# Performance work log

Measured on AMD Instinct MI355X. Metric: run time of the kernel, lower is better.

The kernel has to match this reference:

```python
import jax, jax.numpy as jnp
import numpy as np

N = 50000   # nodes
E = 640000  # edges
IN, H, OUT = 128, 128, 64
BN_EPS = 1e-5


def setup_inputs() -> dict:
    key = jax.random.key(0)
    ks = jax.random.split(key, 16)
    inp = {}
    inp["x"] = jax.random.normal(ks[0], (N, IN), jnp.float32)
    inp["edge_index"] = jax.random.randint(ks[1], (2, E), 0, N, dtype=jnp.int32)
    # BatchNorm affine params (nontrivial so grads are informative)
    inp["bn_in_gamma"] = 1.0 + 0.1 * jax.random.normal(ks[2], (IN,), jnp.float32)
    inp["bn_in_beta"] = 0.1 * jax.random.normal(ks[3], (IN,), jnp.float32)
    inp["bn1_gamma"] = 1.0 + 0.1 * jax.random.normal(ks[4], (H,), jnp.float32)
    inp["bn1_beta"] = 0.1 * jax.random.normal(ks[5], (H,), jnp.float32)
    inp["bn2_gamma"] = 1.0 + 0.1 * jax.random.normal(ks[6], (OUT,), jnp.float32)
    inp["bn2_beta"] = 0.1 * jax.random.normal(ks[7], (OUT,), jnp.float32)
    # Linear / GCNConv weights (fan-in scaled)
    inp["proj_W"] = jax.random.normal(ks[8], (IN, H), jnp.float32) / np.sqrt(IN)
    inp["proj_b"] = jnp.zeros((H,), jnp.float32)
    inp["conv1_W"] = jax.random.normal(ks[9], (H, H), jnp.float32) / np.sqrt(H)
    inp["conv1_b"] = jnp.zeros((H,), jnp.float32)
    inp["conv2_W"] = jax.random.normal(ks[10], (H, OUT), jnp.float32) / np.sqrt(H)
    inp["conv2_b"] = jnp.zeros((OUT,), jnp.float32)
    return inp


def batchnorm(x, gamma, beta):
    # training-mode BN: batch statistics (biased variance), per-feature affine
    m = jnp.mean(x, axis=0)
    v = jnp.mean(jnp.square(x - m), axis=0)
    return (x - m) * jax.lax.rsqrt(v + BN_EPS) * gamma + beta


def gcn_conv(x, src, dst, W, b):
    # PyG GCNConv: y = D^{-1/2} (A + I) D^{-1/2} (x W) + b
    xw = x @ W                                    # [N, F_out]
    loops = jnp.arange(N, dtype=src.dtype)
    s = jnp.concatenate([src, loops])             # [E + N]
    d = jnp.concatenate([dst, loops])
    deg = jax.ops.segment_sum(jnp.ones_like(d, jnp.float32), d, num_segments=N)
    dinv = jnp.where(deg > 0, jax.lax.rsqrt(deg), 0.0)
    norm = dinv[s] * dinv[d]                      # [E + N]
    msgs = xw[s] * norm[:, None]                  # gather + per-edge scale
    out = jax.ops.segment_sum(msgs, d, num_segments=N)  # scatter-add
    return out + b


def reference(x, edge_index, bn_in_gamma, bn_in_beta, bn1_gamma, bn1_beta,
              bn2_gamma, bn2_beta, proj_W, proj_b, conv1_W, conv1_b,
              conv2_W, conv2_b):
    src, dst = edge_index[0], edge_index[1]
    h = batchnorm(x, bn_in_gamma, bn_in_beta)
    h = jax.nn.relu(h @ proj_W + proj_b)
    h = jax.nn.relu(batchnorm(gcn_conv(h, src, dst, conv1_W, conv1_b),
                              bn1_gamma, bn1_beta))
    # dropout: identity in eval mode
    out = batchnorm(gcn_conv(h, src, dst, conv2_W, conv2_b),
                    bn2_gamma, bn2_beta)
    return out
```

## Files before the change

### kernel.cpp

```cpp
#include <hip/hip_runtime.h>

#define NN 50000
#define NE 640000
#define BNEPS 1e-5f
#define NBANK 16
#define CAP 64

#define OFF_DINV 0
#define OFF_CURSOR 51200
#define OFF_ESRC 102400
#define OFF_WT0 1702400
#define OFF_WT1 1710592
#define OFF_WT2 1718784
#define OFF_STATS 1726976
#define OFF_B0 1737216
#define OFF_B1 8137216

typedef __attribute__((ext_vector_type(8))) __bf16 bf16x8;
typedef __attribute__((ext_vector_type(4))) float f32x4;

__device__ __forceinline__ float uplo(unsigned int u) {
  unsigned int v = u << 16;
  return __builtin_bit_cast(float, v);
}
__device__ __forceinline__ float uphi(unsigned int u) {
  unsigned int v = u & 0xffff0000u;
  return __builtin_bit_cast(float, v);
}
__device__ __forceinline__ unsigned int f2bf(float f) {
  unsigned int u = __builtin_bit_cast(unsigned int, f);
  return (u + 0x7fffu + ((u >> 16) & 1u)) >> 16;
}

__global__ __launch_bounds__(256) void prep_k(
    const float* __restrict__ W0, const float* __restrict__ W1,
    const float* __restrict__ W2, unsigned short* __restrict__ T0,
    unsigned short* __restrict__ T1, unsigned short* __restrict__ T2,
    int* __restrict__ cursor, float* __restrict__ stats) {
  const int bid = blockIdx.x;
  const int tid = threadIdx.x;
  if (bid < 160) {
    int f = bid * 256 + tid;
    if (f < 16384) {
      int k = f >> 7, n = f & 127;
      T0[n * 128 + k] = (unsigned short)f2bf(W0[f]);
    } else if (f < 32768) {
      int g = f - 16384;
      int k = g >> 7, n = g & 127;
      T1[n * 128 + k] = (unsigned short)f2bf(W1[g]);
    } else if (f < 40960) {
      int g = f - 32768;
      int k = g >> 6, n = g & 63;
      T2[n * 128 + k] = (unsigned short)f2bf(W2[g]);
    }
  } else if (bid < 356) {
    int i = (bid - 160) * 256 + tid;
    if (i < NN) cursor[i] = i * CAP;
  } else {
    int j = (bid - 356) * 256 + tid;
    stats[j] = 0.0f;
  }
}

template <int NC>
__device__ __forceinline__ void bn_stats_body(
    int sbid, int nsb, int tid, const float* __restrict__ A,
    float* __restrict__ sums, float* __restrict__ sqs, float (*rs)[NC],
    float (*rq)[NC]) {
  constexpr int CG = NC / 4;
  constexpr int RG = 256 / CG;
  const int tc = tid % CG;
  const int tr = tid / CG;
  float s0 = 0, s1 = 0, s2 = 0, s3 = 0, q0 = 0, q1 = 0, q2 = 0, q3 = 0;
  const int stride = nsb * RG;
  for (int r = sbid * RG + tr; r < NN; r += stride) {
    float4 v = *(const float4*)&A[(size_t)r * NC + tc * 4];
    s0 += v.x; s1 += v.y; s2 += v.z; s3 += v.w;
    q0 += v.x * v.x; q1 += v.y * v.y; q2 += v.z * v.z; q3 += v.w * v.w;
  }
  rs[tr][tc * 4] = s0; rs[tr][tc * 4 + 1] = s1;
  rs[tr][tc * 4 + 2] = s2; rs[tr][tc * 4 + 3] = s3;
  rq[tr][tc * 4] = q0; rq[tr][tc * 4 + 1] = q1;
  rq[tr][tc * 4 + 2] = q2; rq[tr][tc * 4 + 3] = q3;
  __syncthreads();
  if (tr == 0) {
    const int bank = (sbid & (NBANK - 1)) * NC;
    for (int j = 0; j < 4; ++j) {
      int c = tc * 4 + j;
      float ts = 0, tq = 0;
      for (int g = 0; g < RG; ++g) { ts += rs[g][c]; tq += rq[g][c]; }
      atomicAdd(&sums[bank + c], ts);
      atomicAdd(&sqs[bank + c], tq);
    }
  }
}

template <int NC>
__global__ __launch_bounds__(256) void bn_stats_k(const float* __restrict__ A,
                                                  float* __restrict__ sums,
                                                  float* __restrict__ sqs) {
  __shared__ float rs[256 / (NC / 4)][NC];
  __shared__ float rq[256 / (NC / 4)][NC];
  bn_stats_body<NC>(blockIdx.x, gridDim.x, threadIdx.x, A, sums, sqs, rs, rq);
}

__global__ __launch_bounds__(256) void bn_stats_bf_k(
    const unsigned short* __restrict__ Z, float* __restrict__ sums,
    float* __restrict__ sqs) {
  const int tc = threadIdx.x % 16;
  const int tr = threadIdx.x / 16;
  const int c = tc * 8;
  float s[8], q[8];
#pragma unroll
  for (int j = 0; j < 8; ++j) { s[j] = 0.f; q[j] = 0.f; }
  const int stride = gridDim.x * 16;
  for (int r = blockIdx.x * 16 + tr; r < NN; r += stride) {
    const uint4 p = *(const uint4*)&Z[(size_t)r * 128 + c];
    float e[8] = {uplo(p.x), uphi(p.x), uplo(p.y), uphi(p.y),
                  uplo(p.z), uphi(p.z), uplo(p.w), uphi(p.w)};
#pragma unroll
    for (int j = 0; j < 8; ++j) { s[j] += e[j]; q[j] += e[j] * e[j]; }
  }
  __shared__ float rs[16][128];
  __shared__ float rq[16][128];
#pragma unroll
  for (int j = 0; j < 8; ++j) { rs[tr][c + j] = s[j]; rq[tr][c + j] = q[j]; }
  __syncthreads();
  if (tr == 0) {
    const int bank = (blockIdx.x & (NBANK - 1)) * 128;
#pragma unroll
    for (int j = 0; j < 8; ++j) {
      float ts = 0.f, tq = 0.f;
      for (int g = 0; g < 16; ++g) { ts += rs[g][c + j]; tq += rq[g][c + j]; }
      atomicAdd(&sums[bank + c + j], ts);
      atomicAdd(&sqs[bank + c + j], tq);
    }
  }
}

template <int NC, int PRE, int EPI>
__device__ __forceinline__ void gemm_body(
    int bid, int tid, char* __restrict__ smem, float* __restrict__ af_s,
    float* __restrict__ bf_s, const void* __restrict__ Ain,
    const unsigned short* __restrict__ Wt, const float* __restrict__ bias,
    const float* __restrict__ sums, const float* __restrict__ sqs,
    const float* __restrict__ gamma, const float* __restrict__ beta,
    unsigned short* __restrict__ O1) {
  constexpr int TM = 64;
  constexpr int NTILES = NC / 16;
  constexpr int CSTR = NC + 4;
  const int row0 = bid * TM;

  if constexpr (PRE != 1) {
    if (tid < 128) {
      float s = 0.f, q = 0.f;
#pragma unroll
      for (int b = 0; b < NBANK; ++b) {
        s += sums[b * 128 + tid];
        q += sqs[b * 128 + tid];
      }
      float m = s * (1.0f / NN);
      float v = q * (1.0f / NN) - m * m;
      float a = gamma[tid] * rsqrtf(v + BNEPS);
      af_s[tid] = a;
      bf_s[tid] = beta[tid] - m * a;
    }
    __syncthreads();
    if constexpr (PRE == 0) {
      const float* A = (const float*)Ain;
      for (int f = tid; f < TM * 32; f += 256) {
        const int r = f >> 5;
        const int c4 = f & 31;
        const int rg = row0 + r;
        float4 v = make_float4(0.f, 0.f, 0.f, 0.f);
        if (rg < NN) {
          v = *(const float4*)&A[(size_t)rg * 128 + c4 * 4];
          const float4 a4 = *(const float4*)&af_s[c4 * 4];
          const float4 b4 = *(const float4*)&bf_s[c4 * 4];
          v.x = fmaf(a4.x, v.x, b4.x);
          v.y = fmaf(a4.y, v.y, b4.y);
          v.z = fmaf(a4.z, v.z, b4.z);
          v.w = fmaf(a4.w, v.w, b4.w);
        }
        uint2 wv;
        wv.x = f2bf(v.x) | (f2bf(v.y) << 16);
        wv.y = f2bf(v.z) | (f2bf(v.w) << 16);
        const int ba = (r * 256 + c4 * 8) ^ ((r & 7) << 4);
        *(uint2*)(smem + ba) = wv;
      }
    } else {
      const unsigned short* Ab = (const unsigned short*)Ain;
      for (int f = tid; f < TM * 16; f += 256) {
        const int r = f >> 4;
        const int c8 = f & 15;
        const int rg = row0 + r;
        uint4 w4 = make_uint4(0u, 0u, 0u, 0u);
        if (rg < NN) {
          const uint4 raw = *(const uint4*)&Ab[(size_t)rg * 128 + c8 * 8];
          const int cc = c8 * 8;
          float e[8] = {uplo(raw.x), uphi(raw.x), uplo(raw.y), uphi(raw.y),
                        uplo(raw.z), uphi(raw.z), uplo(raw.w), uphi(raw.w)};
          unsigned int p[4];
#pragma unroll
          for (int j = 0; j < 4; ++j) {
            float lo =
                fmaxf(fmaf(af_s[cc + 2 * j], e[2 * j], bf_s[cc + 2 * j]), 0.f);
            float hi = fmaxf(
                fmaf(af_s[cc + 2 * j + 1], e[2 * j + 1], bf_s[cc + 2 * j + 1]),
                0.f);
            p[j] = f2bf(lo) | (f2bf(hi) << 16);
          }
          w4 = make_uint4(p[0], p[1], p[2], p[3]);
        }
        const int ba = (r * 256 + c8 * 16) ^ ((r & 7) << 4);
        *(uint4*)(smem + ba) = w4;
      }
    }
    __syncthreads();
  }

  const int w = tid >> 6;
  const int l = tid & 63;
  const int lr = l & 15;
  const int lg = l >> 4;
  f32x4 acc[NTILES];
#pragma unroll
  for (int i = 0; i < NTILES; ++i) acc[i] = (f32x4){0.f, 0.f, 0.f, 0.f};
  const int arow = w * 16 + lr;
#pragma unroll
  for (int kt = 0; kt < 4; ++kt) {
    bf16x8 a;
    if constexpr (PRE == 1) {
      const unsigned short* Ab = (const unsigned short*)Ain;
      a = __builtin_bit_cast(
          bf16x8,
          *(const uint4*)&Ab[(size_t)(row0 + arow) * 128 + kt * 32 + lg * 8]);
    } else {
      const int ba = (arow * 256 + kt * 64 + lg * 16) ^ ((arow & 7) << 4);
      a = __builtin_bit_cast(bf16x8, *(const uint4*)(smem + ba));
    }
#pragma unroll
    for (int nt = 0; nt < NTILES; ++nt) {
      bf16x8 b = __builtin_bit_cast(
          bf16x8,
          *(const uint4*)&Wt[(size_t)(nt * 16 + lr) * 128 + kt * 32 + lg * 8]);
      acc[nt] = __builtin_amdgcn_mfma_f32_16x16x32_bf16(a, b, acc[nt], 0, 0, 0);
    }
  }

  float* Cl = (float*)smem;
  constexpr int CG = NC / 4;
  constexpr int RPH = CG / 8;
  const int tcx = tid % CG;
  const int trx = tid / CG;
  float4 b4 = make_float4(0.f, 0.f, 0.f, 0.f);
  if constexpr (EPI == 0) b4 = *(const float4*)&bias[tcx * 4];
#pragma unroll
  for (int half = 0; half < 2; ++half) {
    __syncthreads();
    if ((w >> 1) == half) {
#pragma unroll
      for (int nt = 0; nt < NTILES; ++nt)
#pragma unroll
        for (int r = 0; r < 4; ++r)
          Cl[((w & 1) * 16 + lg * 4 + r) * CSTR + nt * 16 + lr] = acc[nt][r];
    }
    __syncthreads();
#pragma unroll
    for (int i = 0; i < RPH; ++i) {
      const int rl = trx * RPH + i;
      const int rg = row0 + half * 32 + rl;
      if (rg < NN) {
        float4 v = *(const float4*)&Cl[rl * CSTR + tcx * 4];
        if (EPI == 0) {
          v.x = fmaxf(v.x + b4.x, 0.f);
          v.y = fmaxf(v.y + b4.y, 0.f);
          v.z = fmaxf(v.z + b4.z, 0.f);
          v.w = fmaxf(v.w + b4.w, 0.f);
        }
        uint2 o;
        o.x = f2bf(v.x) | (f2bf(v.y) << 16);
        o.y = f2bf(v.z) | (f2bf(v.w) << 16);
        *(uint2*)&O1[(size_t)rg * NC + tcx * 4] = o;
      }
    }
  }
}

__global__ __launch_bounds__(256) void stats_fill_k(
    const float* __restrict__ x, float* __restrict__ s0,
    float* __restrict__ q0, const int* __restrict__ src,
    const int* __restrict__ dst, int* __restrict__ cursor,
    unsigned short* __restrict__ esrc) {
  __shared__ float rs[8][128];
  __shared__ float rq[8][128];
  const int bid = blockIdx.x;
  if (bid < 1024) {
    bn_stats_body<128>(bid, 1024, threadIdx.x, x, s0, q0, rs, rq);
  } else {
    int e = (bid - 1024) * 256 + threadIdx.x;
    if (e < NE / 2) {
      int p = atomicAdd(&cursor[dst[e]], 1);
      esrc[p] = (unsigned short)src[e];
    }
  }
}

__global__ __launch_bounds__(256) void gemm1_fill_k(
    const float* __restrict__ x, const unsigned short* __restrict__ Wt0,
    const float* __restrict__ proj_b, const float* __restrict__ s0,
    const float* __restrict__ q0, const float* __restrict__ g0,
    const float* __restrict__ b0, unsigned short* __restrict__ H1bf,
    const int* __restrict__ src, const int* __restrict__ dst,
    int* __restrict__ cursor, unsigned short* __restrict__ esrc) {
  __shared__ __align__(16) char smem[17408];
  __shared__ float af_s[128];
  __shared__ float bf_s[128];
  const int bid = blockIdx.x;
  const int tid = threadIdx.x;
  if (bid < 782) {
    gemm_body<128, 0, 0>(bid, tid, smem, af_s, bf_s, x, Wt0, proj_b, s0, q0,
                         g0, b0, H1bf);
  } else {
    int e = NE / 2 + (bid - 782) * 256 + tid;
    if (e < NE) {
      int p = atomicAdd(&cursor[dst[e]], 1);
      esrc[p] = (unsigned short)src[e];
    }
  }
}

__global__ __launch_bounds__(256) void conv1_dinv_k(
    const unsigned short* __restrict__ H1bf,
    const unsigned short* __restrict__ Wt1, unsigned short* __restrict__ Ybf,
    const int* __restrict__ cursor, float* __restrict__ dinv) {
  __shared__ __align__(16) char smem[17408];
  __shared__ float af_s[128];
  __shared__ float bf_s[128];
  const int bid = blockIdx.x;
  const int tid = threadIdx.x;
  if (bid < 782) {
    gemm_body<128, 1, 2>(bid, tid, smem, af_s, bf_s, H1bf, Wt1, nullptr,
                         nullptr, nullptr, nullptr, nullptr, Ybf);
  } else {
    int i = (bid - 782) * 256 + tid;
    if (i < NN) {
      int d = cursor[i] - i * CAP;
      dinv[i] = rsqrtf((float)d + 1.0f);
    }
  }
}

template <int NC, int OUTBF>
__global__ __launch_bounds__(256) void gather_bf_k(
    const int* __restrict__ cursor, const unsigned short* __restrict__ esrc,
    const unsigned short* __restrict__ Y, const float* __restrict__ dinv,
    void* __restrict__ outp, const float* __restrict__ cb) {
  constexpr int CG = NC / 8;
  constexpr int RG = 256 / CG;
  const int tc = threadIdx.x % CG;
  const int tr = threadIdx.x / CG;
  const int n = blockIdx.x * RG + tr;
  if (n >= NN) return;
  const int c = tc * 8;
  const float dn = dinv[n];
  float a[8];
  {
    const uint4 p = *(const uint4*)&Y[(size_t)n * NC + c];
    a[0] = dn * uplo(p.x); a[1] = dn * uphi(p.x);
    a[2] = dn * uplo(p.y); a[3] = dn * uphi(p.y);
    a[4] = dn * uplo(p.z); a[5] = dn * uphi(p.z);
    a[6] = dn * uplo(p.w); a[7] = dn * uphi(p.w);
  }
  const int beg = n * CAP;
  const int end = cursor[n];
  int e = beg;
  for (; e + 2 <= end; e += 2) {
    const int s0 = esrc[e];
    const int s1 = esrc[e + 1];
    const float d0 = dinv[s0];
    const float d1 = dinv[s1];
    const uint4 q0 = *(const uint4*)&Y[(size_t)s0 * NC + c];
    const uint4 q1 = *(const uint4*)&Y[(size_t)s1 * NC + c];
    a[0] = fmaf(d0, uplo(q0.x), a[0]); a[1] = fmaf(d0, uphi(q0.x), a[1]);
    a[2] = fmaf(d0, uplo(q0.y), a[2]); a[3] = fmaf(d0, uphi(q0.y), a[3]);
    a[4] = fmaf(d0, uplo(q0.z), a[4]); a[5] = fmaf(d0, uphi(q0.z), a[5]);
    a[6] = fmaf(d0, uplo(q0.w), a[6]); a[7] = fmaf(d0, uphi(q0.w), a[7]);
    a[0] = fmaf(d1, uplo(q1.x), a[0]); a[1] = fmaf(d1, uphi(q1.x), a[1]);
    a[2] = fmaf(d1, uplo(q1.y), a[2]); a[3] = fmaf(d1, uphi(q1.y), a[3]);
    a[4] = fmaf(d1, uplo(q1.z), a[4]); a[5] = fmaf(d1, uphi(q1.z), a[5]);
    a[6] = fmaf(d1, uplo(q1.w), a[6]); a[7] = fmaf(d1, uphi(q1.w), a[7]);
  }
  if (e < end) {
    const int s0 = esrc[e];
    const float d0 = dinv[s0];
    const uint4 q0 = *(const uint4*)&Y[(size_t)s0 * NC + c];
    a[0] = fmaf(d0, uplo(q0.x), a[0]); a[1] = fmaf(d0, uphi(q0.x), a[1]);
    a[2] = fmaf(d0, uplo(q0.y), a[2]); a[3] = fmaf(d0, uphi(q0.y), a[3]);
    a[4] = fmaf(d0, uplo(q0.z), a[4]); a[5] = fmaf(d0, uphi(q0.z), a[5]);
    a[6] = fmaf(d0, uplo(q0.w), a[6]); a[7] = fmaf(d0, uphi(q0.w), a[7]);
  }
  float z[8];
#pragma unroll
  for (int j = 0; j < 8; ++j) z[j] = fmaf(dn, a[j], cb[c + j]);
  if constexpr (OUTBF == 1) {
    unsigned int p[4];
#pragma unroll
    for (int j = 0; j < 4; ++j)
      p[j] = f2bf(z[2 * j]) | (f2bf(z[2 * j + 1]) << 16);
    *(uint4*)&((unsigned short*)outp)[(size_t)n * NC + c] =
        make_uint4(p[0], p[1], p[2], p[3]);
  } else {
    float* Z = (float*)outp;
    *(float4*)&Z[(size_t)n * NC + c] = make_float4(z[0], z[1], z[2], z[3]);
    *(float4*)&Z[(size_t)n * NC + c + 4] = make_float4(z[4], z[5], z[6], z[7]);
  }
}

template <int NC, int PRE, int EPI>
__global__ __launch_bounds__(256) void mfma_gemm_k(
    const void* __restrict__ Ain, const unsigned short* __restrict__ Wt,
    const float* __restrict__ bias, const float* __restrict__ sums,
    const float* __restrict__ sqs, const float* __restrict__ gamma,
    const float* __restrict__ beta, unsigned short* __restrict__ O1) {
  constexpr int CBYTES = 32 * (NC + 4) * 4;
  constexpr int SMEM = (CBYTES > 16384) ? CBYTES : 16384;
  __shared__ __align__(16) char smem[SMEM];
  __shared__ float af_s[128];
  __shared__ float bf_s[128];
  gemm_body<NC, PRE, EPI>(blockIdx.x, threadIdx.x, smem, af_s, bf_s, Ain, Wt,
                          bias, sums, sqs, gamma, beta, O1);
}

__global__ __launch_bounds__(256) void final_k(
    const float* __restrict__ Z2, const float* __restrict__ s2,
    const float* __restrict__ q2, const float* __restrict__ gamma,
    const float* __restrict__ beta, float* __restrict__ out) {
  __shared__ float af_s[64];
  __shared__ float bf_s[64];
  if (threadIdx.x < 64) {
    float s = 0.f, q = 0.f;
#pragma unroll
    for (int b = 0; b < NBANK; ++b) {
      s += s2[b * 64 + threadIdx.x];
      q += q2[b * 64 + threadIdx.x];
    }
    float m = s * (1.0f / NN);
    float v = q * (1.0f / NN) - m * m;
    float a = gamma[threadIdx.x] * rsqrtf(v + BNEPS);
    af_s[threadIdx.x] = a;
    bf_s[threadIdx.x] = beta[threadIdx.x] - m * a;
  }
  __syncthreads();
  const int u = blockIdx.x * 256 + threadIdx.x;
  if (u >= NN * 16) return;
  const int r = u >> 4;
  const int c = (u & 15) * 4;
  float4 v = *(const float4*)&Z2[(size_t)r * 64 + c];
  const float4 a4 = *(const float4*)&af_s[c];
  const float4 b4 = *(const float4*)&bf_s[c];
  float4 o;
  o.x = fmaf(a4.x, v.x, b4.x);
  o.y = fmaf(a4.y, v.y, b4.y);
  o.z = fmaf(a4.z, v.z, b4.z);
  o.w = fmaf(a4.w, v.w, b4.w);
  *(float4*)&out[(size_t)r * 64 + c] = o;
}

extern "C" void kernel_launch(void* const* d_in, const int* in_sizes, int n_in,
                              void* d_out, int out_size, void* d_ws,
                              size_t ws_size, hipStream_t stream) {
  const float* x = (const float*)d_in[0];
  const int* ei = (const int*)d_in[1];
  const int* src = ei;
  const int* dst = ei + NE;
  const float* bn_in_g = (const float*)d_in[2];
  const float* bn_in_b = (const float*)d_in[3];
  const float* bn1_g = (const float*)d_in[4];
  const float* bn1_b = (const float*)d_in[5];
  const float* bn2_g = (const float*)d_in[6];
  const float* bn2_b = (const float*)d_in[7];
  const float* proj_W = (const float*)d_in[8];
  const float* proj_b = (const float*)d_in[9];
  const float* conv1_W = (const float*)d_in[10];
  const float* conv1_b = (const float*)d_in[11];
  const float* conv2_W = (const float*)d_in[12];
  const float* conv2_b = (const float*)d_in[13];
  float* out = (float*)d_out;

  float* ws = (float*)d_ws;
  float* dinv = ws + OFF_DINV;
  int* cursor = (int*)(ws + OFF_CURSOR);
  unsigned short* esrc = (unsigned short*)(ws + OFF_ESRC);
  unsigned short* Wt0 = (unsigned short*)(ws + OFF_WT0);
  unsigned short* Wt1 = (unsigned short*)(ws + OFF_WT1);
  unsigned short* Wt2 = (unsigned short*)(ws + OFF_WT2);
  float* st = ws + OFF_STATS;
  float* s0 = st;
  float* q0 = st + 2048;
  float* s1 = st + 4096;
  float* q1 = st + 6144;
  float* s2 = st + 8192;
  float* q2 = st + 9216;
  float* B0 = ws + OFF_B0;
  float* B1 = ws + OFF_B1;
  unsigned short* H1bf = (unsigned short*)B0;
  unsigned short* Ybf = (unsigned short*)B1;
  unsigned short* Z1bf = (unsigned short*)B0;
  unsigned short* Y2bf = (unsigned short*)B1;
  float* Z2 = B0;

  prep_k<<<396, 256, 0, stream>>>(proj_W, conv1_W, conv2_W, Wt0, Wt1, Wt2,
                                  cursor, st);
  stats_fill_k<<<2274, 256, 0, stream>>>(x, s0, q0, src, dst, cursor, esrc);
  gemm1_fill_k<<<2032, 256, 0, stream>>>(x, Wt0, proj_b, s0, q0, bn_in_g,
                                         bn_in_b, H1bf, src, dst, cursor, esrc);
  conv1_dinv_k<<<978, 256, 0, stream>>>(H1bf, Wt1, Ybf, cursor, dinv);
  gather_bf_k<128, 1><<<(NN + 15) / 16, 256, 0, stream>>>(cursor, esrc, Ybf,
                                                          dinv, Z1bf, conv1_b);
  bn_stats_bf_k<<<1024, 256, 0, stream>>>(Z1bf, s1, q1);
  mfma_gemm_k<64, 3, 2><<<782, 256, 0, stream>>>(Z1bf, Wt2, nullptr, s1, q1,
                                                 bn1_g, bn1_b, Y2bf);
  gather_bf_k<64, 0><<<(NN + 31) / 32, 256, 0, stream>>>(cursor, esrc, Y2bf,
                                                         dinv, Z2, conv2_b);
  bn_stats_k<64><<<1024, 256, 0, stream>>>(Z2, s2, q2);
  final_k<<<(NN * 16 + 255) / 256, 256, 0, stream>>>(Z2, s2, q2, bn2_g, bn2_b,
                                                     out);
}
```

Baseline: 176.8 us.

## Fuse projection and conv1 GEMMs in one kernel, compute dinv on the fly

```diff
diff --git a/kernel.cpp b/kernel.cpp
--- a/kernel.cpp
+++ b/kernel.cpp
@@ -6,7 +6,6 @@
 #define NBANK 16
 #define CAP 64
 
-#define OFF_DINV 0
 #define OFF_CURSOR 51200
 #define OFF_ESRC 102400
 #define OFF_WT0 1702400
@@ -138,155 +137,6 @@
   }
 }
 
-template <int NC, int PRE, int EPI>
-__device__ __forceinline__ void gemm_body(
-    int bid, int tid, char* __restrict__ smem, float* __restrict__ af_s,
-    float* __restrict__ bf_s, const void* __restrict__ Ain,
-    const unsigned short* __restrict__ Wt, const float* __restrict__ bias,
-    const float* __restrict__ sums, const float* __restrict__ sqs,
-    const float* __restrict__ gamma, const float* __restrict__ beta,
-    unsigned short* __restrict__ O1) {
-  constexpr int TM = 64;
-  constexpr int NTILES = NC / 16;
-  constexpr int CSTR = NC + 4;
-  const int row0 = bid * TM;
-
-  if constexpr (PRE != 1) {
-    if (tid < 128) {
-      float s = 0.f, q = 0.f;
-#pragma unroll
-      for (int b = 0; b < NBANK; ++b) {
-        s += sums[b * 128 + tid];
-        q += sqs[b * 128 + tid];
-      }
-      float m = s * (1.0f / NN);
-      float v = q * (1.0f / NN) - m * m;
-      float a = gamma[tid] * rsqrtf(v + BNEPS);
-      af_s[tid] = a;
-      bf_s[tid] = beta[tid] - m * a;
-    }
-    __syncthreads();
-    if constexpr (PRE == 0) {
-      const float* A = (const float*)Ain;
-      for (int f = tid; f < TM * 32; f += 256) {
-        const int r = f >> 5;
-        const int c4 = f & 31;
-        const int rg = row0 + r;
-        float4 v = make_float4(0.f, 0.f, 0.f, 0.f);
-        if (rg < NN) {
-          v = *(const float4*)&A[(size_t)rg * 128 + c4 * 4];
-          const float4 a4 = *(const float4*)&af_s[c4 * 4];
-          const float4 b4 = *(const float4*)&bf_s[c4 * 4];
-          v.x = fmaf(a4.x, v.x, b4.x);
-          v.y = fmaf(a4.y, v.y, b4.y);
-          v.z = fmaf(a4.z, v.z, b4.z);
-          v.w = fmaf(a4.w, v.w, b4.w);
-        }
-        uint2 wv;
-        wv.x = f2bf(v.x) | (f2bf(v.y) << 16);
-        wv.y = f2bf(v.z) | (f2bf(v.w) << 16);
-        const int ba = (r * 256 + c4 * 8) ^ ((r & 7) << 4);
-        *(uint2*)(smem + ba) = wv;
-      }
-    } else {
-      const unsigned short* Ab = (const unsigned short*)Ain;
-      for (int f = tid; f < TM * 16; f += 256) {
-        const int r = f >> 4;
-        const int c8 = f & 15;
-        const int rg = row0 + r;
-        uint4 w4 = make_uint4(0u, 0u, 0u, 0u);
-        if (rg < NN) {
-          const uint4 raw = *(const uint4*)&Ab[(size_t)rg * 128 + c8 * 8];
-          const int cc = c8 * 8;
-          float e[8] = {uplo(raw.x), uphi(raw.x), uplo(raw.y), uphi(raw.y),
-                        uplo(raw.z), uphi(raw.z), uplo(raw.w), uphi(raw.w)};
-          unsigned int p[4];
-#pragma unroll
-          for (int j = 0; j < 4; ++j) {
-            float lo =
-                fmaxf(fmaf(af_s[cc + 2 * j], e[2 * j], bf_s[cc + 2 * j]), 0.f);
-            float hi = fmaxf(
-                fmaf(af_s[cc + 2 * j + 1], e[2 * j + 1], bf_s[cc + 2 * j + 1]),
-                0.f);
-            p[j] = f2bf(lo) | (f2bf(hi) << 16);
-          }
-          w4 = make_uint4(p[0], p[1], p[2], p[3]);
-        }
-        const int ba = (r * 256 + c8 * 16) ^ ((r & 7) << 4);
-        *(uint4*)(smem + ba) = w4;
-      }
-    }
-    __syncthreads();
-  }
-
-  const int w = tid >> 6;
-  const int l = tid & 63;
-  const int lr = l & 15;
-  const int lg = l >> 4;
-  f32x4 acc[NTILES];
-#pragma unroll
-  for (int i = 0; i < NTILES; ++i) acc[i] = (f32x4){0.f, 0.f, 0.f, 0.f};
-  const int arow = w * 16 + lr;
-#pragma unroll
-  for (int kt = 0; kt < 4; ++kt) {
-    bf16x8 a;
-    if constexpr (PRE == 1) {
-      const unsigned short* Ab = (const unsigned short*)Ain;
-      a = __builtin_bit_cast(
-          bf16x8,
-          *(const uint4*)&Ab[(size_t)(row0 + arow) * 128 + kt * 32 + lg * 8]);
-    } else {
-      const int ba = (arow * 256 + kt * 64 + lg * 16) ^ ((arow & 7) << 4);
-      a = __builtin_bit_cast(bf16x8, *(const uint4*)(smem + ba));
-    }
-#pragma unroll
-    for (int nt = 0; nt < NTILES; ++nt) {
-      bf16x8 b = __builtin_bit_cast(
-          bf16x8,
-          *(const uint4*)&Wt[(size_t)(nt * 16 + lr) * 128 + kt * 32 + lg * 8]);
-      acc[nt] = __builtin_amdgcn_mfma_f32_16x16x32_bf16(a, b, acc[nt], 0, 0, 0);
-    }
-  }
-
-  float* Cl = (float*)smem;
-  constexpr int CG = NC / 4;
-  constexpr int RPH = CG / 8;
-  const int tcx = tid % CG;
-  const int trx = tid / CG;
-  float4 b4 = make_float4(0.f, 0.f, 0.f, 0.f);
-  if constexpr (EPI == 0) b4 = *(const float4*)&bias[tcx * 4];
-#pragma unroll
-  for (int half = 0; half < 2; ++half) {
-    __syncthreads();
-    if ((w >> 1) == half) {
-#pragma unroll
-      for (int nt = 0; nt < NTILES; ++nt)
-#pragma unroll
-        for (int r = 0; r < 4; ++r)
-          Cl[((w & 1) * 16 + lg * 4 + r) * CSTR + nt * 16 + lr] = acc[nt][r];
-    }
-    __syncthreads();
-#pragma unroll
-    for (int i = 0; i < RPH; ++i) {
-      const int rl = trx * RPH + i;
-      const int rg = row0 + half * 32 + rl;
-      if (rg < NN) {
-        float4 v = *(const float4*)&Cl[rl * CSTR + tcx * 4];
-        if (EPI == 0) {
-          v.x = fmaxf(v.x + b4.x, 0.f);
-          v.y = fmaxf(v.y + b4.y, 0.f);
-          v.z = fmaxf(v.z + b4.z, 0.f);
-          v.w = fmaxf(v.w + b4.w, 0.f);
-        }
-        uint2 o;
-        o.x = f2bf(v.x) | (f2bf(v.y) << 16);
-        o.y = f2bf(v.z) | (f2bf(v.w) << 16);
-        *(uint2*)&O1[(size_t)rg * NC + tcx * 4] = o;
-      }
-    }
-  }
-}
-
 __global__ __launch_bounds__(256) void stats_fill_k(
     const float* __restrict__ x, float* __restrict__ s0,
     float* __restrict__ q0, const int* __restrict__ src,
@@ -306,47 +156,140 @@
   }
 }
 
-__global__ __launch_bounds__(256) void gemm1_fill_k(
+__global__ __launch_bounds__(256) void fused12_fill_k(
     const float* __restrict__ x, const unsigned short* __restrict__ Wt0,
-    const float* __restrict__ proj_b, const float* __restrict__ s0,
-    const float* __restrict__ q0, const float* __restrict__ g0,
-    const float* __restrict__ b0, unsigned short* __restrict__ H1bf,
-    const int* __restrict__ src, const int* __restrict__ dst,
-    int* __restrict__ cursor, unsigned short* __restrict__ esrc) {
+    const unsigned short* __restrict__ Wt1, const float* __restrict__ proj_b,
+    const float* __restrict__ s0, const float* __restrict__ q0,
+    const float* __restrict__ g0, const float* __restrict__ b0,
+    unsigned short* __restrict__ Ybf, const int* __restrict__ src,
+    const int* __restrict__ dst, int* __restrict__ cursor,
+    unsigned short* __restrict__ esrc) {
   __shared__ __align__(16) char smem[17408];
   __shared__ float af_s[128];
   __shared__ float bf_s[128];
+  __shared__ float pb_s[128];
   const int bid = blockIdx.x;
   const int tid = threadIdx.x;
-  if (bid < 782) {
-    gemm_body<128, 0, 0>(bid, tid, smem, af_s, bf_s, x, Wt0, proj_b, s0, q0,
-                         g0, b0, H1bf);
-  } else {
+  if (bid >= 782) {
     int e = NE / 2 + (bid - 782) * 256 + tid;
     if (e < NE) {
       int p = atomicAdd(&cursor[dst[e]], 1);
       esrc[p] = (unsigned short)src[e];
     }
-  }
-}
-
-__global__ __launch_bounds__(256) void conv1_dinv_k(
-    const unsigned short* __restrict__ H1bf,
-    const unsigned short* __restrict__ Wt1, unsigned short* __restrict__ Ybf,
-    const int* __restrict__ cursor, float* __restrict__ dinv) {
-  __shared__ __align__(16) char smem[17408];
-  __shared__ float af_s[128];
-  __shared__ float bf_s[128];
-  const int bid = blockIdx.x;
-  const int tid = threadIdx.x;
-  if (bid < 782) {
-    gemm_body<128, 1, 2>(bid, tid, smem, af_s, bf_s, H1bf, Wt1, nullptr,
-                         nullptr, nullptr, nullptr, nullptr, Ybf);
-  } else {
-    int i = (bid - 782) * 256 + tid;
-    if (i < NN) {
-      int d = cursor[i] - i * CAP;
-      dinv[i] = rsqrtf((float)d + 1.0f);
+    return;
+  }
+  const int row0 = bid * 64;
+  if (tid < 128) {
+    float s = 0.f, q = 0.f;
+#pragma unroll
+    for (int b = 0; b < NBANK; ++b) {
+      s += s0[b * 128 + tid];
+      q += q0[b * 128 + tid];
+    }
+    float m = s * (1.0f / NN);
+    float v = q * (1.0f / NN) - m * m;
+    float a = g0[tid] * rsqrtf(v + BNEPS);
+    af_s[tid] = a;
+    bf_s[tid] = b0[tid] - m * a;
+    pb_s[tid] = proj_b[tid];
+  }
+  __syncthreads();
+  for (int f = tid; f < 64 * 32; f += 256) {
+    const int r = f >> 5;
+    const int c4 = f & 31;
+    const int rg = row0 + r;
+    float4 v = make_float4(0.f, 0.f, 0.f, 0.f);
+    if (rg < NN) {
+      v = *(const float4*)&x[(size_t)rg * 128 + c4 * 4];
+      const float4 a4 = *(const float4*)&af_s[c4 * 4];
+      const float4 b4 = *(const float4*)&bf_s[c4 * 4];
+      v.x = fmaf(a4.x, v.x, b4.x);
+      v.y = fmaf(a4.y, v.y, b4.y);
+      v.z = fmaf(a4.z, v.z, b4.z);
+      v.w = fmaf(a4.w, v.w, b4.w);
+    }
+    uint2 wv;
+    wv.x = f2bf(v.x) | (f2bf(v.y) << 16);
+    wv.y = f2bf(v.z) | (f2bf(v.w) << 16);
+    const int ba = (r * 256 + c4 * 8) ^ ((r & 7) << 4);
+    *(uint2*)(smem + ba) = wv;
+  }
+  __syncthreads();
+
+  const int w = tid >> 6;
+  const int l = tid & 63;
+  const int lr = l & 15;
+  const int lg = l >> 4;
+  const int arow = w * 16 + lr;
+  f32x4 acc[8];
+#pragma unroll
+  for (int i = 0; i < 8; ++i) acc[i] = (f32x4){0.f, 0.f, 0.f, 0.f};
+#pragma unroll
+  for (int kt = 0; kt < 4; ++kt) {
+    const int ba = (arow * 256 + kt * 64 + lg * 16) ^ ((arow & 7) << 4);
+    bf16x8 a = __builtin_bit_cast(bf16x8, *(const uint4*)(smem + ba));
+#pragma unroll
+    for (int nt = 0; nt < 8; ++nt) {
+      bf16x8 b = __builtin_bit_cast(
+          bf16x8,
+          *(const uint4*)&Wt0[(size_t)(nt * 16 + lr) * 128 + kt * 32 + lg * 8]);
+      acc[nt] = __builtin_amdgcn_mfma_f32_16x16x32_bf16(a, b, acc[nt], 0, 0, 0);
+    }
+  }
+  __syncthreads();
+#pragma unroll
+  for (int nt = 0; nt < 8; ++nt) {
+    const float pb = pb_s[nt * 16 + lr];
+#pragma unroll
+    for (int r = 0; r < 4; ++r) {
+      const int row = w * 16 + lg * 4 + r;
+      const float hv = fmaxf(acc[nt][r] + pb, 0.f);
+      const int ba = (row * 256 + (nt * 16 + lr) * 2) ^ ((row & 7) << 4);
+      *(unsigned short*)(smem + ba) = (unsigned short)f2bf(hv);
+    }
+  }
+  __syncthreads();
+  f32x4 acc2[8];
+#pragma unroll
+  for (int i = 0; i < 8; ++i) acc2[i] = (f32x4){0.f, 0.f, 0.f, 0.f};
+#pragma unroll
+  for (int kt = 0; kt < 4; ++kt) {
+    const int ba = (arow * 256 + kt * 64 + lg * 16) ^ ((arow & 7) << 4);
+    bf16x8 a = __builtin_bit_cast(bf16x8, *(const uint4*)(smem + ba));
+#pragma unroll
+    for (int nt = 0; nt < 8; ++nt) {
+      bf16x8 b = __builtin_bit_cast(
+          bf16x8,
+          *(const uint4*)&Wt1[(size_t)(nt * 16 + lr) * 128 + kt * 32 + lg * 8]);
+      acc2[nt] =
+          __builtin_amdgcn_mfma_f32_16x16x32_bf16(a, b, acc2[nt], 0, 0, 0);
+    }
+  }
+  float* Cl = (float*)smem;
+  const int tcx = tid % 32;
+  const int trx = tid / 32;
+#pragma unroll
+  for (int half = 0; half < 2; ++half) {
+    __syncthreads();
+    if ((w >> 1) == half) {
+#pragma unroll
+      for (int nt = 0; nt < 8; ++nt)
+#pragma unroll
+        for (int r = 0; r < 4; ++r)
+          Cl[((w & 1) * 16 + lg * 4 + r) * 132 + nt * 16 + lr] = acc2[nt][r];
+    }
+    __syncthreads();
+#pragma unroll
+    for (int i = 0; i < 4; ++i) {
+      const int rl = trx * 4 + i;
+      const int rg = row0 + half * 32 + rl;
+      if (rg < NN) {
+        float4 v = *(const float4*)&Cl[rl * 132 + tcx * 4];
+        uint2 o;
+        o.x = f2bf(v.x) | (f2bf(v.y) << 16);
+        o.y = f2bf(v.z) | (f2bf(v.w) << 16);
+        *(uint2*)&Ybf[(size_t)rg * 128 + tcx * 4] = o;
+      }
     }
   }
 }
@@ -354,8 +297,8 @@
 template <int NC, int OUTBF>
 __global__ __launch_bounds__(256) void gather_bf_k(
     const int* __restrict__ cursor, const unsigned short* __restrict__ esrc,
-    const unsigned short* __restrict__ Y, const float* __restrict__ dinv,
-    void* __restrict__ outp, const float* __restrict__ cb) {
+    const unsigned short* __restrict__ Y, void* __restrict__ outp,
+    const float* __restrict__ cb) {
   constexpr int CG = NC / 8;
   constexpr int RG = 256 / CG;
   const int tc = threadIdx.x % CG;
@@ -363,7 +306,9 @@
   const int n = blockIdx.x * RG + tr;
   if (n >= NN) return;
   const int c = tc * 8;
-  const float dn = dinv[n];
+  const int beg = n * CAP;
+  const int end = cursor[n];
+  const float dn = rsqrtf((float)(end - beg) + 1.0f);
   float a[8];
   {
     const uint4 p = *(const uint4*)&Y[(size_t)n * NC + c];
@@ -372,14 +317,12 @@
     a[4] = dn * uplo(p.z); a[5] = dn * uphi(p.z);
     a[6] = dn * uplo(p.w); a[7] = dn * uphi(p.w);
   }
-  const int beg = n * CAP;
-  const int end = cursor[n];
   int e = beg;
   for (; e + 2 <= end; e += 2) {
     const int s0 = esrc[e];
     const int s1 = esrc[e + 1];
-    const float d0 = dinv[s0];
-    const float d1 = dinv[s1];
+    const float d0 = rsqrtf((float)(cursor[s0] - s0 * CAP) + 1.0f);
+    const float d1 = rsqrtf((float)(cursor[s1] - s1 * CAP) + 1.0f);
     const uint4 q0 = *(const uint4*)&Y[(size_t)s0 * NC + c];
     const uint4 q1 = *(const uint4*)&Y[(size_t)s1 * NC + c];
     a[0] = fmaf(d0, uplo(q0.x), a[0]); a[1] = fmaf(d0, uphi(q0.x), a[1]);
@@ -393,7 +336,7 @@
   }
   if (e < end) {
     const int s0 = esrc[e];
-    const float d0 = dinv[s0];
+    const float d0 = rsqrtf((float)(cursor[s0] - s0 * CAP) + 1.0f);
     const uint4 q0 = *(const uint4*)&Y[(size_t)s0 * NC + c];
     a[0] = fmaf(d0, uplo(q0.x), a[0]); a[1] = fmaf(d0, uphi(q0.x), a[1]);
     a[2] = fmaf(d0, uplo(q0.y), a[2]); a[3] = fmaf(d0, uphi(q0.y), a[3]);
@@ -417,19 +360,101 @@
   }
 }
 
-template <int NC, int PRE, int EPI>
-__global__ __launch_bounds__(256) void mfma_gemm_k(
-    const void* __restrict__ Ain, const unsigned short* __restrict__ Wt,
-    const float* __restrict__ bias, const float* __restrict__ sums,
-    const float* __restrict__ sqs, const float* __restrict__ gamma,
-    const float* __restrict__ beta, unsigned short* __restrict__ O1) {
-  constexpr int CBYTES = 32 * (NC + 4) * 4;
-  constexpr int SMEM = (CBYTES > 16384) ? CBYTES : 16384;
-  __shared__ __align__(16) char smem[SMEM];
+__global__ __launch_bounds__(256) void conv2_k(
+    const unsigned short* __restrict__ Z1, const unsigned short* __restrict__ Wt,
+    const float* __restrict__ sums, const float* __restrict__ sqs,
+    const float* __restrict__ gamma, const float* __restrict__ beta,
+    unsigned short* __restrict__ O1) {
+  __shared__ __align__(16) char smem[16384];
   __shared__ float af_s[128];
   __shared__ float bf_s[128];
-  gemm_body<NC, PRE, EPI>(blockIdx.x, threadIdx.x, smem, af_s, bf_s, Ain, Wt,
-                          bias, sums, sqs, gamma, beta, O1);
+  const int tid = threadIdx.x;
+  const int row0 = blockIdx.x * 64;
+  if (tid < 128) {
+    float s = 0.f, q = 0.f;
+#pragma unroll
+    for (int b = 0; b < NBANK; ++b) {
+      s += sums[b * 128 + tid];
+      q += sqs[b * 128 + tid];
+    }
+    float m = s * (1.0f / NN);
+    float v = q * (1.0f / NN) - m * m;
+    float a = gamma[tid] * rsqrtf(v + BNEPS);
+    af_s[tid] = a;
+    bf_s[tid] = beta[tid] - m * a;
+  }
+  __syncthreads();
+  for (int f = tid; f < 64 * 16; f += 256) {
+    const int r = f >> 4;
+    const int c8 = f & 15;
+    const int rg = row0 + r;
+    uint4 w4 = make_uint4(0u, 0u, 0u, 0u);
+    if (rg < NN) {
+      const uint4 raw = *(const uint4*)&Z1[(size_t)rg * 128 + c8 * 8];
+      const int cc = c8 * 8;
+      float e[8] = {uplo(raw.x), uphi(raw.x), uplo(raw.y), uphi(raw.y),
+                    uplo(raw.z), uphi(raw.z), uplo(raw.w), uphi(raw.w)};
+      unsigned int p[4];
+#pragma unroll
+      for (int j = 0; j < 4; ++j) {
+        float lo = fmaxf(fmaf(af_s[cc + 2 * j], e[2 * j], bf_s[cc + 2 * j]), 0.f);
+        float hi = fmaxf(
+            fmaf(af_s[cc + 2 * j + 1], e[2 * j + 1], bf_s[cc + 2 * j + 1]), 0.f);
+        p[j] = f2bf(lo) | (f2bf(hi) << 16);
+      }
+      w4 = make_uint4(p[0], p[1], p[2], p[3]);
+    }
+    const int ba = (r * 256 + c8 * 16) ^ ((r & 7) << 4);
+    *(uint4*)(smem + ba) = w4;
+  }
+  __syncthreads();
+  const int w = tid >> 6;
+  const int l = tid & 63;
+  const int lr = l & 15;
+  const int lg = l >> 4;
+  const int arow = w * 16 + lr;
+  f32x4 acc[4];
+#pragma unroll
+  for (int i = 0; i < 4; ++i) acc[i] = (f32x4){0.f, 0.f, 0.f, 0.f};
+#pragma unroll
+  for (int kt = 0; kt < 4; ++kt) {
+    const int ba = (arow * 256 + kt * 64 + lg * 16) ^ ((arow & 7) << 4);
+    bf16x8 a = __builtin_bit_cast(bf16x8, *(const uint4*)(smem + ba));
+#pragma unroll
+    for (int nt = 0; nt < 4; ++nt) {
+      bf16x8 b = __builtin_bit_cast(
+          bf16x8,
+          *(const uint4*)&Wt[(size_t)(nt * 16 + lr) * 128 + kt * 32 + lg * 8]);
+      acc[nt] = __builtin_amdgcn_mfma_f32_16x16x32_bf16(a, b, acc[nt], 0, 0, 0);
+    }
+  }
+  float* Cl = (float*)smem;
+  const int tcx = tid % 16;
+  const int trx = tid / 16;
+#pragma unroll
+  for (int half = 0; half < 2; ++half) {
+    __syncthreads();
+    if ((w >> 1) == half) {
+#pragma unroll
+      for (int nt = 0; nt < 4; ++nt)
+#pragma unroll
+        for (int r = 0; r < 4; ++r)
+          Cl[((w & 1) * 16 + lg * 4 + r) * 68 + nt * 16 + lr] = acc[nt][r];
+    }
+    __syncthreads();
+#pragma unroll
+    for (int i = 0; i < 2; ++i) {
+      const int rl = trx * 2 + i;
+      const int rg = row0 + half * 32 + rl;
+      if (rg < NN) {
+        float4 v = *(const float4*)&Cl[rl * 68 + tcx * 4];
+        uint2 o;
+        o.x = f2bf(v.x) | (f2bf(v.y) << 16);
+        o.y = f2bf(v.z) | (f2bf(v.w) << 16);
+        *(uint2*)&O1[(size_t)rg * 64 + tcx * 4] = o;
+      }
+    }
+  }
 }
 
 __global__ __launch_bounds__(256) void final_k(
@@ -489,7 +514,6 @@
   float* out = (float*)d_out;
 
   float* ws = (float*)d_ws;
-  float* dinv = ws + OFF_DINV;
   int* cursor = (int*)(ws + OFF_CURSOR);
   unsigned short* esrc = (unsigned short*)(ws + OFF_ESRC);
   unsigned short* Wt0 = (unsigned short*)(ws + OFF_WT0);
@@ -504,7 +528,6 @@
   float* q2 = st + 9216;
   float* B0 = ws + OFF_B0;
   float* B1 = ws + OFF_B1;
-  unsigned short* H1bf = (unsigned short*)B0;
   unsigned short* Ybf = (unsigned short*)B1;
   unsigned short* Z1bf = (unsigned short*)B0;
   unsigned short* Y2bf = (unsigned short*)B1;
@@ -513,16 +536,15 @@
   prep_k<<<396, 256, 0, stream>>>(proj_W, conv1_W, conv2_W, Wt0, Wt1, Wt2,
                                   cursor, st);
   stats_fill_k<<<2274, 256, 0, stream>>>(x, s0, q0, src, dst, cursor, esrc);
-  gemm1_fill_k<<<2032, 256, 0, stream>>>(x, Wt0, proj_b, s0, q0, bn_in_g,
-                                         bn_in_b, H1bf, src, dst, cursor, esrc);
-  conv1_dinv_k<<<978, 256, 0, stream>>>(H1bf, Wt1, Ybf, cursor, dinv);
+  fused12_fill_k<<<2032, 256, 0, stream>>>(x, Wt0, Wt1, proj_b, s0, q0,
+                                           bn_in_g, bn_in_b, Ybf, src, dst,
+                                           cursor, esrc);
   gather_bf_k<128, 1><<<(NN + 15) / 16, 256, 0, stream>>>(cursor, esrc, Ybf,
-                                                          dinv, Z1bf, conv1_b);
+                                                          Z1bf, conv1_b);
   bn_stats_bf_k<<<1024, 256, 0, stream>>>(Z1bf, s1, q1);
-  mfma_gemm_k<64, 3, 2><<<782, 256, 0, stream>>>(Z1bf, Wt2, nullptr, s1, q1,
-                                                 bn1_g, bn1_b, Y2bf);
+  conv2_k<<<782, 256, 0, stream>>>(Z1bf, Wt2, s1, q1, bn1_g, bn1_b, Y2bf);
   gather_bf_k<64, 0><<<(NN + 31) / 32, 256, 0, stream>>>(cursor, esrc, Y2bf,
-                                                         dinv, Z2, conv2_b);
+                                                         Z2, conv2_b);
   bn_stats_k<64><<<1024, 256, 0, stream>>>(Z2, s2, q2);
   final_k<<<(NN * 16 + 255) / 256, 256, 0, stream>>>(Z2, s2, q2, bn2_g, bn2_b,
                                                      out);
```

Measured after the change: 169.1 us. 1.05x faster.
